# Performance work log

Measured on AMD Instinct MI355X. Metric: run time of the kernel, lower is better.

The kernel has to match this reference:

```python
import jax, jax.numpy as jnp
import numpy as np
from jax import lax

DN = ('NCHW', 'OIHW', 'NCHW')

def conv(x, w, pad='VALID'):
    return lax.conv_general_dilated(x, w, (1, 1), pad, dimension_numbers=DN)

def adaptive_matrix(in_s, out_s):
    # exact torch adaptive_avg_pool2d bin weights: start=floor(i*in/out), end=ceil((i+1)*in/out)
    M = np.zeros((out_s, in_s), np.float32)
    for i in range(out_s):
        s = (i * in_s) // out_s
        e = -(-((i + 1) * in_s) // out_s)
        M[i, s:e] = 1.0 / (e - s)
    return jnp.asarray(M)

def setup_inputs() -> dict:
    key = jax.random.key(0)
    ks = jax.random.split(key, 11)
    C = 64
    def w(k, shape, fan_in):
        return jax.random.normal(k, shape, jnp.float32) * (1.0 / np.sqrt(fan_in))
    return {
        'x': jax.random.normal(ks[0], (16, C, 128, 128), jnp.float32),
        'conv1_w': w(ks[1], (2 * C, C, 1, 1), C),
        'conv1_b': jnp.zeros((2 * C,), jnp.float32),
        'conv2_w': w(ks[2], (C, C, 1, 1), C),
        'conv2_b': jnp.zeros((C,), jnp.float32),
        'conv3_w': w(ks[3], (C, 2 * C, 1, 1), 2 * C),
        'conv3_b': jnp.zeros((C,), jnp.float32),
        'pos_w': w(ks[4], (C, C, 3, 3), C * 9),
        'pos_b': jnp.zeros((C,), jnp.float32),
        'se_w1': w(ks[5], (C // 8, C, 1, 1), C),
        'se_w2': w(ks[6], (C, C // 8, 1, 1), C // 8),
    }

def reference(x, conv1_w, conv1_b, conv2_w, conv2_b, conv3_w, conv3_b, pos_w, pos_b, se_w1, se_w2):
    C, nw, ext = 64, 4, 4
    y = conv(x, conv1_w) + conv1_b[None, :, None, None]
    x1, x2 = y[:, :C], y[:, C:]
    N, _, H, W = x1.shape
    x1p = jnp.pad(x1, ((0, 0), (0, 0), (ext, ext), (ext, ext)), mode='edge')
    Hp, Wp = H + 2 * ext, W + 2 * ext
    Hs, Ws = H // nw, W // nw
    Hk, Wk = Hs + H % nw, Ws + W % nw
    Hps, Wps = Hp // nw, Wp // nw
    Hpk, Wpk = Hps + Hp % nw, Wps + Wp % nw
    # unfold: windows row-major (h_window fastest over j), shape (N, nw^2, C, Hpk, Wpk)
    wins = jnp.stack([x1p[:, :, i * Hps:i * Hps + Hpk, j * Wps:j * Wps + Wpk]
                      for i in range(nw) for j in range(nw)], axis=1)
    Ph = adaptive_matrix(Hpk, Hk)
    Pw = adaptive_matrix(Wpk, Wk)
    pooled = jnp.einsum('nlchw,Hh,Ww->nlcHW', wins, Ph, Pw).reshape(N * nw * nw, C, Hk, Wk)
    pr = (conv(pooled, conv2_w) + conv2_b[None, :, None, None]
          + conv(pooled, pos_w, 'SAME') + pos_b[None, :, None, None])
    # SE attention
    s = jnp.mean(pr, axis=(2, 3), keepdims=True)
    s = jax.nn.sigmoid(conv(jax.nn.relu(conv(s, se_w1)), se_w2))
    att = pr * s + pr
    # faithful torch .view(N, C*Hk*Wk, nw^2) memory reinterpretation, then fold
    cols = att.reshape(N, nw * nw * C * Hk * Wk).reshape(N, C, Hk, Wk, nw * nw)
    out = jnp.zeros((N, C, H, W), x.dtype)
    cnt = jnp.zeros((N, 1, H, W), x.dtype)
    for i in range(nw):
        for j in range(nw):
            l = i * nw + j
            out = out.at[:, :, i * Hs:i * Hs + Hk, j * Ws:j * Ws + Wk].add(cols[..., l])
            cnt = cnt.at[:, :, i * Hs:i * Hs + Hk, j * Ws:j * Ws + Wk].add(1.0)
    out = out / cnt
    return conv(jnp.concatenate([out, x2], axis=1), conv3_w) + conv3_b[None, :, None, None]
```

## Files before the change

kernel.cpp:

```cpp
#include <hip/hip_runtime.h>

constexpr int N = 16, C = 64, H = 128, W = 128, P = H * W;
constexpr int NL = 256, PK = 1024;

constexpr size_t OFF_RA    = 0;
constexpr size_t OFF_RB    = 8388608;
constexpr size_t OFF_RC    = 16777216;
constexpr size_t OFF_SUMS  = 33554432;
constexpr size_t OFF_SCALE = OFF_SUMS  + 16384;
constexpr size_t OFF_WMOD  = OFF_SCALE + 16384;
constexpr size_t OFF_W1L   = OFF_WMOD  + 18432;
constexpr size_t OFF_W3L   = OFF_W1L   + 4096;

typedef short bf16x8 __attribute__((ext_vector_type(8)));
typedef float f32x4  __attribute__((ext_vector_type(4)));

__device__ inline unsigned short f2bf(float f) {
    unsigned u = __float_as_uint(f);
    unsigned r = (u + 0x7FFFu + ((u >> 16) & 1u)) >> 16;
    return (unsigned short)r;
}
__device__ inline float bf2f(unsigned short h) {
    return __uint_as_float(((unsigned)h) << 16);
}

__global__ __launch_bounds__(256) void k0_prep(const float* __restrict__ pos_w,
                                               const float* __restrict__ conv2_w,
                                               const float* __restrict__ w1,
                                               const float* __restrict__ w3,
                                               unsigned short* __restrict__ wmod,
                                               unsigned short* __restrict__ w1lay,
                                               unsigned short* __restrict__ w3lay,
                                               float* __restrict__ sums) {
    int t = blockIdx.x * 256 + threadIdx.x;
    if (t < 36864) {
        int cir = t & 31;
        int co  = (t >> 5) & 63;
        int cib = (t >> 11) & 1;
        int tap = t >> 12;
        int ci  = cib * 32 + cir;
        float v = pos_w[(co * 64 + ci) * 9 + tap];
        if (tap == 4) v += conv2_w[co * 64 + ci];
        wmod[t] = f2bf(v);
    } else if (t < 45056) {
        int u = t - 36864;
        int cir = u & 31;
        int co  = (u >> 5) & 127;
        int cib = u >> 12;
        w1lay[u] = f2bf(w1[co * 64 + cib * 32 + cir]);
    } else if (t < 53248) {
        int u = t - 45056;
        int cir = u & 31;
        int co  = (u >> 5) & 63;
        int cib = u >> 11;
        w3lay[u] = f2bf(w3[co * 128 + cib * 32 + cir]);
    } else {
        sums[t - 53248] = 0.f;
    }
}

__global__ __launch_bounds__(256) void k1_conv1(const float* __restrict__ x,
                                                const unsigned short* __restrict__ w1lay,
                                                const float* __restrict__ b1,
                                                unsigned short* __restrict__ x1t,
                                                unsigned short* __restrict__ xcat) {
    __shared__ __align__(16) float lda[64 * 65];
    __shared__ __align__(16) unsigned short ldb[128 * 64];
    int bid = blockIdx.x;
    int n   = bid >> 7;
    int px0 = (bid & 127) << 7;
    int t   = threadIdx.x;
    #pragma unroll
    for (int s = 0; s < 2; ++s) {
        if (s) __syncthreads();
        const float* src = x + (size_t)n * 64 * P + px0 + s * 64;
        #pragma unroll
        for (int k = 0; k < 4; ++k) {
            int u = t + k * 256;
            int ci = u >> 4, px4 = u & 15;
            float4 v = *(const float4*)(src + (size_t)ci * P + px4 * 4);
            float* d = lda + ci * 65 + px4 * 4;
            d[0] = v.x; d[1] = v.y; d[2] = v.z; d[3] = v.w;
        }
        __syncthreads();
        int cig = t & 15, pxl = t >> 4;
        #pragma unroll
        for (int k = 0; k < 4; ++k) {
            int px = pxl + k * 16;
            ushort4 o;
            o.x = f2bf(lda[(cig * 4 + 0) * 65 + px]);
            o.y = f2bf(lda[(cig * 4 + 1) * 65 + px]);
            o.z = f2bf(lda[(cig * 4 + 2) * 65 + px]);
            o.w = f2bf(lda[(cig * 4 + 3) * 65 + px]);
            int pg = s * 64 + px;
            int chunk = cig >> 1;
            *(ushort4*)(ldb + pg * 64 + ((chunk ^ (pg & 7)) * 8) + (cig & 1) * 4) = o;
        }
    }
    __syncthreads();
    int wave = t >> 6, lane = t & 63;
    int quad = lane >> 4, l16 = lane & 15;
    int pxw = wave * 32;
    f32x4 acc[8][2] = {};
    #pragma unroll
    for (int cib = 0; cib < 2; ++cib) {
        bf16x8 af[8], bfr[2];
        #pragma unroll
        for (int ct = 0; ct < 8; ++ct)
            af[ct] = *(const bf16x8*)(w1lay + ((size_t)(cib * 128 + ct * 16 + l16)) * 32 + quad * 8);
        #pragma unroll
        for (int pt = 0; pt < 2; ++pt) {
            int pg = pxw + pt * 16 + l16;
            int chunk = cib * 4 + quad;
            bfr[pt] = *(const bf16x8*)(ldb + pg * 64 + ((chunk ^ (pg & 7)) * 8));
        }
        #pragma unroll
        for (int ct = 0; ct < 8; ++ct)
            #pragma unroll
            for (int pt = 0; pt < 2; ++pt)
                acc[ct][pt] = __builtin_amdgcn_mfma_f32_16x16x32_bf16(af[ct], bfr[pt], acc[ct][pt], 0, 0, 0);
    }
    #pragma unroll
    for (int ct = 0; ct < 8; ++ct) {
        int co0 = ct * 16 + quad * 4;
        float4 bb = *(const float4*)(b1 + co0);
        #pragma unroll
        for (int pt = 0; pt < 2; ++pt) {
            int px = px0 + pxw + pt * 16 + l16;
            ushort4 o;
            o.x = f2bf(acc[ct][pt][0] + bb.x);
            o.y = f2bf(acc[ct][pt][1] + bb.y);
            o.z = f2bf(acc[ct][pt][2] + bb.z);
            o.w = f2bf(acc[ct][pt][3] + bb.w);
            if (co0 < 64)
                *(ushort4*)(x1t + ((size_t)n * P + px) * 64 + co0) = o;
            else
                *(ushort4*)(xcat + ((size_t)n * P + px) * 128 + co0) = o;
        }
    }
}

__global__ __launch_bounds__(256) void k3_pool_pr(const unsigned short* __restrict__ x1t,
                                                  const unsigned short* __restrict__ wmod,
                                                  const float* __restrict__ b2,
                                                  const float* __restrict__ posb,
                                                  unsigned short* __restrict__ prb,
                                                  float* __restrict__ sums) {
    __shared__ __align__(16) unsigned short lxs[340 * 32];
    int bid = blockIdx.x;
    int nl  = bid >> 2;
    int r0  = (bid & 3) * 8;
    int n   = nl >> 4, wl = nl & 15;
    int wi  = wl >> 2, wj = wl & 3;
    int t   = threadIdx.x;
    const unsigned short* xb = x1t + (size_t)n * P * 64;
    int wave = t >> 6, lane = t & 63;
    int quad = lane >> 4, l16 = lane & 15;
    int wrow0 = wave * 2;
    f32x4 acc[4][4] = {};
    #pragma unroll
    for (int cib = 0; cib < 2; ++cib) {
        if (cib) __syncthreads();
        for (int it = 0; it < 6; ++it) {
            int e = t + it * 256;
            if (e < 1360) {
                int pix = e >> 2, part = e & 3;
                int lr = pix / 34, lc = pix - lr * 34;
                int gr = r0 - 1 + lr, gc = lc - 1;
                unsigned short oc[8];
                if ((unsigned)gr < 32u && (unsigned)gc < 32u) {
                    int sh = gr + (gr >> 4), sw = gc + (gc >> 4);
                    int u = wi * 34 + sh - 4, v = wj * 34 + sw - 4;
                    int ra = min(max(u, 0), 127), rb = min(max(u + 1, 0), 127);
                    int ca = min(max(v, 0), 127), cb = min(max(v + 1, 0), 127);
                    int off = cib * 32 + part * 8;
                    uint4 A = *(const uint4*)(xb + (size_t)(ra * 128 + ca) * 64 + off);
                    uint4 B = *(const uint4*)(xb + (size_t)(ra * 128 + cb) * 64 + off);
                    uint4 Cc = *(const uint4*)(xb + (size_t)(rb * 128 + ca) * 64 + off);
                    uint4 D = *(const uint4*)(xb + (size_t)(rb * 128 + cb) * 64 + off);
                    const unsigned short* a = (const unsigned short*)&A;
                    const unsigned short* b = (const unsigned short*)&B;
                    const unsigned short* c = (const unsigned short*)&Cc;
                    const unsigned short* d = (const unsigned short*)&D;
                    #pragma unroll
                    for (int q = 0; q < 8; ++q)
                        oc[q] = f2bf(0.25f * (bf2f(a[q]) + bf2f(b[q]) + bf2f(c[q]) + bf2f(d[q])));
                } else {
                    #pragma unroll
                    for (int q = 0; q < 8; ++q) oc[q] = 0;
                }
                *(uint4*)(lxs + pix * 32 + ((part ^ ((pix >> 1) & 3)) * 8)) = *(const uint4*)oc;
            }
        }
        __syncthreads();
        #pragma unroll
        for (int tap = 0; tap < 9; ++tap) {
            int dh = tap / 3, dw = tap % 3;
            bf16x8 af[4], bfr[4];
            #pragma unroll
            for (int ct = 0; ct < 4; ++ct)
                af[ct] = *(const bf16x8*)(wmod + (((tap * 2 + cib) * 64) + ct * 16 + l16) * 32 + quad * 8);
            #pragma unroll
            for (int pt = 0; pt < 4; ++pt) {
                int pix = (wrow0 + (pt >> 1) + dh) * 34 + ((pt & 1) * 16 + l16 + dw);
                bfr[pt] = *(const bf16x8*)(lxs + pix * 32 + ((quad ^ ((pix >> 1) & 3)) * 8));
            }
            #pragma unroll
            for (int ct = 0; ct < 4; ++ct)
                #pragma unroll
                for (int pt = 0; pt < 4; ++pt)
                    acc[ct][pt] = __builtin_amdgcn_mfma_f32_16x16x32_bf16(af[ct], bfr[pt], acc[ct][pt], 0, 0, 0);
        }
    }
    #pragma unroll
    for (int ct = 0; ct < 4; ++ct) {
        #pragma unroll
        for (int r = 0; r < 4; ++r) {
            int co = ct * 16 + quad * 4 + r;
            float bias = b2[co] + posb[co];
            float s = 0.f;
            #pragma unroll
            for (int pt = 0; pt < 4; ++pt) {
                float v = acc[ct][pt][r] + bias;
                int row = r0 + wrow0 + (pt >> 1);
                int col = (pt & 1) * 16 + l16;
                prb[(size_t)nl * 65536 + co * 1024 + row * 32 + col] = f2bf(v);
                s += v;
            }
            s += __shfl_xor(s, 1);
            s += __shfl_xor(s, 2);
            s += __shfl_xor(s, 4);
            s += __shfl_xor(s, 8);
            if (l16 == 0) atomicAdd(&sums[nl * 64 + co], s);
        }
    }
}

__global__ __launch_bounds__(64) void k3b_se(const float* __restrict__ sums,
                                             const float* __restrict__ w1,
                                             const float* __restrict__ w2,
                                             float* __restrict__ scale) {
    __shared__ float m[64];
    __shared__ float hid[8];
    int nl = blockIdx.x;
    int t  = threadIdx.x;
    m[t] = sums[nl * 64 + t] * (1.f / 1024.f);
    __syncthreads();
    if (t < 8) {
        float s = 0.f;
        #pragma unroll
        for (int ci = 0; ci < 64; ++ci) s += w1[t * 64 + ci] * m[ci];
        hid[t] = fmaxf(s, 0.f);
    }
    __syncthreads();
    float v = 0.f;
    #pragma unroll
    for (int r = 0; r < 8; ++r) v += w2[t * 8 + r] * hid[r];
    scale[nl * 64 + t] = 1.f + 1.f / (1.f + __expf(-v));
}

__global__ __launch_bounds__(256) void k4_unscramble(const unsigned short* __restrict__ prb,
                                                     const float* __restrict__ scale,
                                                     unsigned short* __restrict__ xcat) {
    int tid = blockIdx.x * 256 + threadIdx.x;
    int cg = tid & 7;
    int w2 = (tid >> 3) & 31;
    int h2 = (tid >> 8) & 31;
    int i  = (tid >> 13) & 3;
    int n  = tid >> 15;
    int hh = (h2 & 1) * 16 + (w2 >> 1);
    int pixbase = hh * 32 + (w2 & 1) * 16 + i * 4;
    unsigned short o[4][8];
    #pragma unroll
    for (int m = 0; m < 8; ++m) {
        int c  = cg * 8 + m;
        int nl = n * 16 + (c >> 2);
        int cc = (c & 3) * 16 + (h2 >> 1);
        ushort4 v = *(const ushort4*)(prb + (size_t)nl * 65536 + cc * 1024 + pixbase);
        float s = scale[nl * 64 + cc];
        o[0][m] = f2bf(bf2f(v.x) * s);
        o[1][m] = f2bf(bf2f(v.y) * s);
        o[2][m] = f2bf(bf2f(v.z) * s);
        o[3][m] = f2bf(bf2f(v.w) * s);
    }
    int H_ = i * 32 + h2;
    #pragma unroll
    for (int j = 0; j < 4; ++j) {
        int W_ = j * 32 + w2;
        *(uint4*)(xcat + ((size_t)n * P + H_ * 128 + W_) * 128 + cg * 8) = *(const uint4*)o[j];
    }
}

__global__ __launch_bounds__(256) void k5_conv3(const unsigned short* __restrict__ xcat,
                                                const unsigned short* __restrict__ w3lay,
                                                const float* __restrict__ b3,
                                                float* __restrict__ out) {
    __shared__ __align__(16) unsigned short lxs[128 * 136];
    int bid = blockIdx.x;
    int n   = bid >> 7;
    int px0 = (bid & 127) << 7;
    const unsigned short* src = xcat + ((size_t)n * P + px0) * 128;
    int t = threadIdx.x;
    #pragma unroll
    for (int it = 0; it < 8; ++it) {
        int e = t + it * 256;
        int pix = e >> 4, part = e & 15;
        *(uint4*)(lxs + pix * 136 + part * 8) = *(const uint4*)(src + pix * 128 + part * 8);
    }
    __syncthreads();
    int wave = t >> 6, lane = t & 63;
    int quad = lane >> 4, l16 = lane & 15;
    int pxw = wave * 32;
    f32x4 acc[4][2] = {};
    #pragma unroll
    for (int cib = 0; cib < 4; ++cib) {
        bf16x8 af[4], bfr[2];
        #pragma unroll
        for (int ct = 0; ct < 4; ++ct)
            af[ct] = *(const bf16x8*)(w3lay + ((size_t)(cib * 64 + ct * 16 + l16)) * 32 + quad * 8);
        #pragma unroll
        for (int pt = 0; pt < 2; ++pt)
            bfr[pt] = *(const bf16x8*)(lxs + (pxw + pt * 16 + l16) * 136 + cib * 32 + quad * 8);
        #pragma unroll
        for (int ct = 0; ct < 4; ++ct)
            #pragma unroll
            for (int pt = 0; pt < 2; ++pt)
                acc[ct][pt] = __builtin_amdgcn_mfma_f32_16x16x32_bf16(af[ct], bfr[pt], acc[ct][pt], 0, 0, 0);
    }
    #pragma unroll
    for (int ct = 0; ct < 4; ++ct) {
        int co0 = ct * 16 + quad * 4;
        float4 bb = *(const float4*)(b3 + co0);
        #pragma unroll
        for (int pt = 0; pt < 2; ++pt) {
            int px = px0 + pxw + pt * 16 + l16;
            const float* bp = (const float*)&bb;
            #pragma unroll
            for (int r = 0; r < 4; ++r)
                out[((size_t)n * 64 + co0 + r) * P + px] = acc[ct][pt][r] + bp[r];
        }
    }
}

extern "C" void kernel_launch(void* const* d_in, const int* in_sizes, int n_in,
                              void* d_out, int out_size, void* d_ws, size_t ws_size,
                              hipStream_t stream) {
    const float* x       = (const float*)d_in[0];
    const float* conv1_w = (const float*)d_in[1];
    const float* conv1_b = (const float*)d_in[2];
    const float* conv2_w = (const float*)d_in[3];
    const float* conv2_b = (const float*)d_in[4];
    const float* conv3_w = (const float*)d_in[5];
    const float* conv3_b = (const float*)d_in[6];
    const float* pos_w   = (const float*)d_in[7];
    const float* pos_b   = (const float*)d_in[8];
    const float* se_w1   = (const float*)d_in[9];
    const float* se_w2   = (const float*)d_in[10];

    float* ws = (float*)d_ws;
    unsigned short* prb  = (unsigned short*)(ws + OFF_RA);
    unsigned short* x1t  = (unsigned short*)(ws + OFF_RB);
    unsigned short* xcat = (unsigned short*)(ws + OFF_RC);
    float* sums  = ws + OFF_SUMS;
    float* scale = ws + OFF_SCALE;
    unsigned short* wmod  = (unsigned short*)(ws + OFF_WMOD);
    unsigned short* w1lay = (unsigned short*)(ws + OFF_W1L);
    unsigned short* w3lay = (unsigned short*)(ws + OFF_W3L);

    k0_prep      <<<272,  256, 0, stream>>>(pos_w, conv2_w, conv1_w, conv3_w,
                                            wmod, w1lay, w3lay, sums);
    k1_conv1     <<<2048, 256, 0, stream>>>(x, w1lay, conv1_b, x1t, xcat);
    k3_pool_pr   <<<1024, 256, 0, stream>>>(x1t, wmod, conv2_b, pos_b, prb, sums);
    k3b_se       <<<256,  64,  0, stream>>>(sums, se_w1, se_w2, scale);
    k4_unscramble<<<2048, 256, 0, stream>>>(prb, scale, xcat);
    k5_conv3     <<<2048, 256, 0, stream>>>(xcat, w3lay, conv3_b, (float*)d_out);
}
```

Baseline: 257.9 us.

## Fuse SE, unscramble and weight prep into neighbouring kernels, cutting launches

Folds weight preparation and sums zeroing into extra blocks of the conv1 kernel. It also fuses the SE scale computation and the fold/unscramble directly into the conv3 kernel, which now gathers the pooled result from prb with scaling instead of going through an xcat buffer. Conv1 now reads x and w1 straight from global memory without LDS staging. The pool kernel stages both channel halves at once with a single barrier. Kernel launches drop from six to three and the xcat round trip is removed, at the cost of uncoalesced scalar gathers in conv1 and conv3 and redundant SE computation per block.

New measurement: 275.1 us. 6.7% more time.

```diff
diff --git a/kernel.cpp b/kernel.cpp
--- a/kernel.cpp
+++ b/kernel.cpp
@@ -3,14 +3,12 @@
 constexpr int N = 16, C = 64, H = 128, W = 128, P = H * W;
 constexpr int NL = 256, PK = 1024;
 
-constexpr size_t OFF_RA    = 0;
-constexpr size_t OFF_RB    = 8388608;
-constexpr size_t OFF_RC    = 16777216;
-constexpr size_t OFF_SUMS  = 33554432;
-constexpr size_t OFF_SCALE = OFF_SUMS  + 16384;
-constexpr size_t OFF_WMOD  = OFF_SCALE + 16384;
-constexpr size_t OFF_W1L   = OFF_WMOD  + 18432;
-constexpr size_t OFF_W3L   = OFF_W1L   + 4096;
+constexpr size_t OFF_RA   = 0;
+constexpr size_t OFF_RB   = 8388608;
+constexpr size_t OFF_RC   = 16777216;
+constexpr size_t OFF_SUMS = 25165824;
+constexpr size_t OFF_WMOD = OFF_SUMS + 16384;
+constexpr size_t OFF_W3L  = OFF_WMOD + 18432;
 
 typedef short bf16x8 __attribute__((ext_vector_type(8)));
 typedef float f32x4  __attribute__((ext_vector_type(4)));
@@ -24,101 +22,67 @@
     return __uint_as_float(((unsigned)h) << 16);
 }
 
-__global__ __launch_bounds__(256) void k0_prep(const float* __restrict__ pos_w,
-                                               const float* __restrict__ conv2_w,
-                                               const float* __restrict__ w1,
-                                               const float* __restrict__ w3,
-                                               unsigned short* __restrict__ wmod,
-                                               unsigned short* __restrict__ w1lay,
-                                               unsigned short* __restrict__ w3lay,
-                                               float* __restrict__ sums) {
-    int t = blockIdx.x * 256 + threadIdx.x;
-    if (t < 36864) {
-        int cir = t & 31;
-        int co  = (t >> 5) & 63;
-        int cib = (t >> 11) & 1;
-        int tap = t >> 12;
-        int ci  = cib * 32 + cir;
-        float v = pos_w[(co * 64 + ci) * 9 + tap];
-        if (tap == 4) v += conv2_w[co * 64 + ci];
-        wmod[t] = f2bf(v);
-    } else if (t < 45056) {
-        int u = t - 36864;
-        int cir = u & 31;
-        int co  = (u >> 5) & 127;
-        int cib = u >> 12;
-        w1lay[u] = f2bf(w1[co * 64 + cib * 32 + cir]);
-    } else if (t < 53248) {
-        int u = t - 45056;
-        int cir = u & 31;
-        int co  = (u >> 5) & 63;
-        int cib = u >> 11;
-        w3lay[u] = f2bf(w3[co * 128 + cib * 32 + cir]);
-    } else {
-        sums[t - 53248] = 0.f;
-    }
-}
-
 __global__ __launch_bounds__(256) void k1_conv1(const float* __restrict__ x,
-                                                const unsigned short* __restrict__ w1lay,
+                                                const float* __restrict__ w1,
                                                 const float* __restrict__ b1,
+                                                const float* __restrict__ pos_w,
+                                                const float* __restrict__ conv2_w,
+                                                const float* __restrict__ w3,
                                                 unsigned short* __restrict__ x1t,
-                                                unsigned short* __restrict__ xcat) {
-    __shared__ __align__(16) float lda[64 * 65];
-    __shared__ __align__(16) unsigned short ldb[128 * 64];
+                                                unsigned short* __restrict__ x2t,
+                                                unsigned short* __restrict__ wmod,
+                                                unsigned short* __restrict__ w3lay,
+                                                float* __restrict__ sums) {
     int bid = blockIdx.x;
-    int n   = bid >> 7;
-    int px0 = (bid & 127) << 7;
     int t   = threadIdx.x;
-    #pragma unroll
-    for (int s = 0; s < 2; ++s) {
-        if (s) __syncthreads();
-        const float* src = x + (size_t)n * 64 * P + px0 + s * 64;
-        #pragma unroll
-        for (int k = 0; k < 4; ++k) {
-            int u = t + k * 256;
-            int ci = u >> 4, px4 = u & 15;
-            float4 v = *(const float4*)(src + (size_t)ci * P + px4 * 4);
-            float* d = lda + ci * 65 + px4 * 4;
-            d[0] = v.x; d[1] = v.y; d[2] = v.z; d[3] = v.w;
-        }
-        __syncthreads();
-        int cig = t & 15, pxl = t >> 4;
-        #pragma unroll
-        for (int k = 0; k < 4; ++k) {
-            int px = pxl + k * 16;
-            ushort4 o;
-            o.x = f2bf(lda[(cig * 4 + 0) * 65 + px]);
-            o.y = f2bf(lda[(cig * 4 + 1) * 65 + px]);
-            o.z = f2bf(lda[(cig * 4 + 2) * 65 + px]);
-            o.w = f2bf(lda[(cig * 4 + 3) * 65 + px]);
-            int pg = s * 64 + px;
-            int chunk = cig >> 1;
-            *(ushort4*)(ldb + pg * 64 + ((chunk ^ (pg & 7)) * 8) + (cig & 1) * 4) = o;
-        }
-    }
-    __syncthreads();
+    if (bid >= 2048) {
+        for (int u = (bid - 2048) * 256 + t; u < 61440; u += 8192) {
+            if (u < 36864) {
+                int cir = u & 31, co = (u >> 5) & 63, cib = (u >> 11) & 1, tap = u >> 12;
+                int ci = cib * 32 + cir;
+                float v = pos_w[(co * 64 + ci) * 9 + tap];
+                if (tap == 4) v += conv2_w[co * 64 + ci];
+                wmod[u] = f2bf(v);
+            } else if (u < 45056) {
+                int q = u - 36864;
+                int cir = q & 31, co = (q >> 5) & 63, cib = q >> 11;
+                w3lay[q] = f2bf(w3[co * 128 + cib * 32 + cir]);
+            } else {
+                sums[u - 45056] = 0.f;
+            }
+        }
+        return;
+    }
+    int n    = bid >> 7;
     int wave = t >> 6, lane = t & 63;
     int quad = lane >> 4, l16 = lane & 15;
-    int pxw = wave * 32;
+    int px0  = (bid & 127) * 128 + wave * 32;
+    const float* xb = x + (size_t)n * 64 * P;
     f32x4 acc[8][2] = {};
     #pragma unroll
     for (int cib = 0; cib < 2; ++cib) {
-        bf16x8 af[8], bfr[2];
-        #pragma unroll
-        for (int ct = 0; ct < 8; ++ct)
-            af[ct] = *(const bf16x8*)(w1lay + ((size_t)(cib * 128 + ct * 16 + l16)) * 32 + quad * 8);
-        #pragma unroll
-        for (int pt = 0; pt < 2; ++pt) {
-            int pg = pxw + pt * 16 + l16;
-            int chunk = cib * 4 + quad;
-            bfr[pt] = *(const bf16x8*)(ldb + pg * 64 + ((chunk ^ (pg & 7)) * 8));
-        }
-        #pragma unroll
-        for (int ct = 0; ct < 8; ++ct)
-            #pragma unroll
-            for (int pt = 0; pt < 2; ++pt)
-                acc[ct][pt] = __builtin_amdgcn_mfma_f32_16x16x32_bf16(af[ct], bfr[pt], acc[ct][pt], 0, 0, 0);
+        bf16x8 bfr[2];
+        #pragma unroll
+        for (int pt = 0; pt < 2; ++pt) {
+            int px = px0 + pt * 16 + l16;
+            unsigned short tmp[8];
+            #pragma unroll
+            for (int j = 0; j < 8; ++j)
+                tmp[j] = f2bf(xb[(size_t)(cib * 32 + quad * 8 + j) * P + px]);
+            bfr[pt] = *(bf16x8*)tmp;
+        }
+        #pragma unroll
+        for (int ct = 0; ct < 8; ++ct) {
+            const float* wr = w1 + (ct * 16 + l16) * 64 + cib * 32 + quad * 8;
+            float4 wa = *(const float4*)wr;
+            float4 wb = *(const float4*)(wr + 4);
+            unsigned short wt[8];
+            wt[0] = f2bf(wa.x); wt[1] = f2bf(wa.y); wt[2] = f2bf(wa.z); wt[3] = f2bf(wa.w);
+            wt[4] = f2bf(wb.x); wt[5] = f2bf(wb.y); wt[6] = f2bf(wb.z); wt[7] = f2bf(wb.w);
+            bf16x8 af = *(bf16x8*)wt;
+            acc[ct][0] = __builtin_amdgcn_mfma_f32_16x16x32_bf16(af, bfr[0], acc[ct][0], 0, 0, 0);
+            acc[ct][1] = __builtin_amdgcn_mfma_f32_16x16x32_bf16(af, bfr[1], acc[ct][1], 0, 0, 0);
+        }
     }
     #pragma unroll
     for (int ct = 0; ct < 8; ++ct) {
@@ -126,7 +90,7 @@
         float4 bb = *(const float4*)(b1 + co0);
         #pragma unroll
         for (int pt = 0; pt < 2; ++pt) {
-            int px = px0 + pxw + pt * 16 + l16;
+            int px = px0 + pt * 16 + l16;
             ushort4 o;
             o.x = f2bf(acc[ct][pt][0] + bb.x);
             o.y = f2bf(acc[ct][pt][1] + bb.y);
@@ -135,7 +99,7 @@
             if (co0 < 64)
                 *(ushort4*)(x1t + ((size_t)n * P + px) * 64 + co0) = o;
             else
-                *(ushort4*)(xcat + ((size_t)n * P + px) * 128 + co0) = o;
+                *(ushort4*)(x2t + ((size_t)n * P + px) * 64 + (co0 - 64)) = o;
         }
     }
 }
@@ -146,7 +110,7 @@
                                                   const float* __restrict__ posb,
                                                   unsigned short* __restrict__ prb,
                                                   float* __restrict__ sums) {
-    __shared__ __align__(16) unsigned short lxs[340 * 32];
+    __shared__ __align__(16) unsigned short lxs[2 * 340 * 32];
     int bid = blockIdx.x;
     int nl  = bid >> 2;
     int r0  = (bid & 3) * 8;
@@ -154,48 +118,50 @@
     int wi  = wl >> 2, wj = wl & 3;
     int t   = threadIdx.x;
     const unsigned short* xb = x1t + (size_t)n * P * 64;
+    for (int it = 0; it < 11; ++it) {
+        int e = t + it * 256;
+        if (e < 2720) {
+            int part = e & 3;
+            int u    = e >> 2;
+            int cib  = (u >= 340);
+            int pix  = u - cib * 340;
+            int lr = pix / 34, lc = pix - lr * 34;
+            int gr = r0 - 1 + lr, gc = lc - 1;
+            unsigned short oc[8];
+            if ((unsigned)gr < 32u && (unsigned)gc < 32u) {
+                int sh = gr + (gr >> 4), sw = gc + (gc >> 4);
+                int uu = wi * 34 + sh - 4, vv = wj * 34 + sw - 4;
+                int ra = min(max(uu, 0), 127), rb = min(max(uu + 1, 0), 127);
+                int ca = min(max(vv, 0), 127), cb = min(max(vv + 1, 0), 127);
+                int off = cib * 32 + part * 8;
+                uint4 A  = *(const uint4*)(xb + (size_t)(ra * 128 + ca) * 64 + off);
+                uint4 B  = *(const uint4*)(xb + (size_t)(ra * 128 + cb) * 64 + off);
+                uint4 Cc = *(const uint4*)(xb + (size_t)(rb * 128 + ca) * 64 + off);
+                uint4 D  = *(const uint4*)(xb + (size_t)(rb * 128 + cb) * 64 + off);
+                const unsigned short* a = (const unsigned short*)&A;
+                const unsigned short* b = (const unsigned short*)&B;
+                const unsigned short* c = (const unsigned short*)&Cc;
+                const unsigned short* d = (const unsigned short*)&D;
+                #pragma unroll
+                for (int q = 0; q < 8; ++q)
+                    oc[q] = f2bf(0.25f * (bf2f(a[q]) + bf2f(b[q]) + bf2f(c[q]) + bf2f(d[q])));
+            } else {
+                #pragma unroll
+                for (int q = 0; q < 8; ++q) oc[q] = 0;
+            }
+            *(uint4*)(lxs + cib * 10880 + pix * 32 + ((part ^ ((pix >> 1) & 3)) * 8)) = *(const uint4*)oc;
+        }
+    }
+    __syncthreads();
     int wave = t >> 6, lane = t & 63;
     int quad = lane >> 4, l16 = lane & 15;
     int wrow0 = wave * 2;
     f32x4 acc[4][4] = {};
     #pragma unroll
-    for (int cib = 0; cib < 2; ++cib) {
-        if (cib) __syncthreads();
-        for (int it = 0; it < 6; ++it) {
-            int e = t + it * 256;
-            if (e < 1360) {
-                int pix = e >> 2, part = e & 3;
-                int lr = pix / 34, lc = pix - lr * 34;
-                int gr = r0 - 1 + lr, gc = lc - 1;
-                unsigned short oc[8];
-                if ((unsigned)gr < 32u && (unsigned)gc < 32u) {
-                    int sh = gr + (gr >> 4), sw = gc + (gc >> 4);
-                    int u = wi * 34 + sh - 4, v = wj * 34 + sw - 4;
-                    int ra = min(max(u, 0), 127), rb = min(max(u + 1, 0), 127);
-                    int ca = min(max(v, 0), 127), cb = min(max(v + 1, 0), 127);
-                    int off = cib * 32 + part * 8;
-                    uint4 A = *(const uint4*)(xb + (size_t)(ra * 128 + ca) * 64 + off);
-                    uint4 B = *(const uint4*)(xb + (size_t)(ra * 128 + cb) * 64 + off);
-                    uint4 Cc = *(const uint4*)(xb + (size_t)(rb * 128 + ca) * 64 + off);
-                    uint4 D = *(const uint4*)(xb + (size_t)(rb * 128 + cb) * 64 + off);
-                    const unsigned short* a = (const unsigned short*)&A;
-                    const unsigned short* b = (const unsigned short*)&B;
-                    const unsigned short* c = (const unsigned short*)&Cc;
-                    const unsigned short* d = (const unsigned short*)&D;
-                    #pragma unroll
-                    for (int q = 0; q < 8; ++q)
-                        oc[q] = f2bf(0.25f * (bf2f(a[q]) + bf2f(b[q]) + bf2f(c[q]) + bf2f(d[q])));
-                } else {
-                    #pragma unroll
-                    for (int q = 0; q < 8; ++q) oc[q] = 0;
-                }
-                *(uint4*)(lxs + pix * 32 + ((part ^ ((pix >> 1) & 3)) * 8)) = *(const uint4*)oc;
-            }
-        }
-        __syncthreads();
-        #pragma unroll
-        for (int tap = 0; tap < 9; ++tap) {
-            int dh = tap / 3, dw = tap % 3;
+    for (int tap = 0; tap < 9; ++tap) {
+        int dh = tap / 3, dw = tap % 3;
+        #pragma unroll
+        for (int cib = 0; cib < 2; ++cib) {
             bf16x8 af[4], bfr[4];
             #pragma unroll
             for (int ct = 0; ct < 4; ++ct)
@@ -203,7 +169,7 @@
             #pragma unroll
             for (int pt = 0; pt < 4; ++pt) {
                 int pix = (wrow0 + (pt >> 1) + dh) * 34 + ((pt & 1) * 16 + l16 + dw);
-                bfr[pt] = *(const bf16x8*)(lxs + pix * 32 + ((quad ^ ((pix >> 1) & 3)) * 8));
+                bfr[pt] = *(const bf16x8*)(lxs + cib * 10880 + pix * 32 + ((quad ^ ((pix >> 1) & 3)) * 8));
             }
             #pragma unroll
             for (int ct = 0; ct < 4; ++ct)
@@ -236,108 +202,96 @@
     }
 }
 
-__global__ __launch_bounds__(64) void k3b_se(const float* __restrict__ sums,
-                                             const float* __restrict__ w1,
-                                             const float* __restrict__ w2,
-                                             float* __restrict__ scale) {
-    __shared__ float m[64];
-    __shared__ float hid[8];
-    int nl = blockIdx.x;
-    int t  = threadIdx.x;
-    m[t] = sums[nl * 64 + t] * (1.f / 1024.f);
-    __syncthreads();
-    if (t < 8) {
-        float s = 0.f;
-        #pragma unroll
-        for (int ci = 0; ci < 64; ++ci) s += w1[t * 64 + ci] * m[ci];
-        hid[t] = fmaxf(s, 0.f);
-    }
-    __syncthreads();
-    float v = 0.f;
-    #pragma unroll
-    for (int r = 0; r < 8; ++r) v += w2[t * 8 + r] * hid[r];
-    scale[nl * 64 + t] = 1.f + 1.f / (1.f + __expf(-v));
-}
-
-__global__ __launch_bounds__(256) void k4_unscramble(const unsigned short* __restrict__ prb,
-                                                     const float* __restrict__ scale,
-                                                     unsigned short* __restrict__ xcat) {
-    int tid = blockIdx.x * 256 + threadIdx.x;
-    int cg = tid & 7;
-    int w2 = (tid >> 3) & 31;
-    int h2 = (tid >> 8) & 31;
-    int i  = (tid >> 13) & 3;
-    int n  = tid >> 15;
-    int hh = (h2 & 1) * 16 + (w2 >> 1);
-    int pixbase = hh * 32 + (w2 & 1) * 16 + i * 4;
-    unsigned short o[4][8];
-    #pragma unroll
-    for (int m = 0; m < 8; ++m) {
-        int c  = cg * 8 + m;
-        int nl = n * 16 + (c >> 2);
-        int cc = (c & 3) * 16 + (h2 >> 1);
-        ushort4 v = *(const ushort4*)(prb + (size_t)nl * 65536 + cc * 1024 + pixbase);
-        float s = scale[nl * 64 + cc];
-        o[0][m] = f2bf(bf2f(v.x) * s);
-        o[1][m] = f2bf(bf2f(v.y) * s);
-        o[2][m] = f2bf(bf2f(v.z) * s);
-        o[3][m] = f2bf(bf2f(v.w) * s);
-    }
-    int H_ = i * 32 + h2;
-    #pragma unroll
-    for (int j = 0; j < 4; ++j) {
-        int W_ = j * 32 + w2;
-        *(uint4*)(xcat + ((size_t)n * P + H_ * 128 + W_) * 128 + cg * 8) = *(const uint4*)o[j];
-    }
-}
-
-__global__ __launch_bounds__(256) void k5_conv3(const unsigned short* __restrict__ xcat,
+__global__ __launch_bounds__(256) void k5_conv3(const unsigned short* __restrict__ prb,
+                                                const float* __restrict__ sums,
+                                                const float* __restrict__ se_w1,
+                                                const float* __restrict__ se_w2,
+                                                const unsigned short* __restrict__ x2t,
                                                 const unsigned short* __restrict__ w3lay,
                                                 const float* __restrict__ b3,
                                                 float* __restrict__ out) {
-    __shared__ __align__(16) unsigned short lxs[128 * 136];
-    int bid = blockIdx.x;
-    int n   = bid >> 7;
-    int px0 = (bid & 127) << 7;
-    const unsigned short* src = xcat + ((size_t)n * P + px0) * 128;
-    int t = threadIdx.x;
-    #pragma unroll
-    for (int it = 0; it < 8; ++it) {
-        int e = t + it * 256;
-        int pix = e >> 4, part = e & 15;
-        *(uint4*)(lxs + pix * 136 + part * 8) = *(const uint4*)(src + pix * 128 + part * 8);
+    __shared__ float shid[16][8];
+    __shared__ float sscale[64];
+    int bid  = blockIdx.x;
+    int n    = bid >> 7;
+    int Hrow = bid & 127;
+    int h2 = Hrow & 31, ib = Hrow >> 5;
+    int t  = threadIdx.x;
+    if (t < 128) {
+        int lam = t >> 3, r = t & 7;
+        const float* sp = sums + (n * 16 + lam) * 64;
+        float s = 0.f;
+        #pragma unroll
+        for (int ci = 0; ci < 64; ++ci) s += se_w1[r * 64 + ci] * sp[ci];
+        shid[lam][r] = fmaxf(s * (1.f / 1024.f), 0.f);
+    }
+    __syncthreads();
+    if (t < 64) {
+        int lam = t >> 2, q = t & 3;
+        int cc = q * 16 + (h2 >> 1);
+        float v = 0.f;
+        #pragma unroll
+        for (int r = 0; r < 8; ++r) v += se_w2[cc * 8 + r] * shid[lam][r];
+        sscale[t] = 1.f + 1.f / (1.f + __expf(-v));
     }
     __syncthreads();
     int wave = t >> 6, lane = t & 63;
     int quad = lane >> 4, l16 = lane & 15;
-    int pxw = wave * 32;
     f32x4 acc[4][2] = {};
     #pragma unroll
-    for (int cib = 0; cib < 4; ++cib) {
-        bf16x8 af[4], bfr[2];
-        #pragma unroll
-        for (int ct = 0; ct < 4; ++ct)
-            af[ct] = *(const bf16x8*)(w3lay + ((size_t)(cib * 64 + ct * 16 + l16)) * 32 + quad * 8);
-        #pragma unroll
-        for (int pt = 0; pt < 2; ++pt)
-            bfr[pt] = *(const bf16x8*)(lxs + (pxw + pt * 16 + l16) * 136 + cib * 32 + quad * 8);
-        #pragma unroll
-        for (int ct = 0; ct < 4; ++ct)
+    for (int cib = 0; cib < 2; ++cib) {
+        bf16x8 bfr[2];
+        #pragma unroll
+        for (int pt = 0; pt < 2; ++pt) {
+            int Wp = wave * 32 + pt * 16 + l16;
+            int w2 = Wp & 31, jW = Wp >> 5;
+            int hh  = (h2 & 1) * 16 + (w2 >> 1);
+            int pix = hh * 32 + (w2 & 1) * 16 + ib * 4 + jW;
+            unsigned short tmp[8];
+            #pragma unroll
+            for (int j = 0; j < 8; ++j) {
+                int c  = cib * 32 + quad * 8 + j;
+                int nl = n * 16 + (c >> 2);
+                int cc = (c & 3) * 16 + (h2 >> 1);
+                tmp[j] = f2bf(bf2f(prb[(size_t)nl * 65536 + cc * 1024 + pix]) * sscale[c]);
+            }
+            bfr[pt] = *(bf16x8*)tmp;
+        }
+        #pragma unroll
+        for (int ct = 0; ct < 4; ++ct) {
+            bf16x8 af = *(const bf16x8*)(w3lay + ((size_t)(cib * 64 + ct * 16 + l16)) * 32 + quad * 8);
             #pragma unroll
             for (int pt = 0; pt < 2; ++pt)
-                acc[ct][pt] = __builtin_amdgcn_mfma_f32_16x16x32_bf16(af[ct], bfr[pt], acc[ct][pt], 0, 0, 0);
+                acc[ct][pt] = __builtin_amdgcn_mfma_f32_16x16x32_bf16(af, bfr[pt], acc[ct][pt], 0, 0, 0);
+        }
+    }
+    #pragma unroll
+    for (int cb = 0; cb < 2; ++cb) {
+        bf16x8 bfr[2];
+        #pragma unroll
+        for (int pt = 0; pt < 2; ++pt) {
+            int Wp = wave * 32 + pt * 16 + l16;
+            bfr[pt] = *(const bf16x8*)(x2t + ((size_t)n * P + Hrow * 128 + Wp) * 64 + cb * 32 + quad * 8);
+        }
+        #pragma unroll
+        for (int ct = 0; ct < 4; ++ct) {
+            bf16x8 af = *(const bf16x8*)(w3lay + ((size_t)((2 + cb) * 64 + ct * 16 + l16)) * 32 + quad * 8);
+            #pragma unroll
+            for (int pt = 0; pt < 2; ++pt)
+                acc[ct][pt] = __builtin_amdgcn_mfma_f32_16x16x32_bf16(af, bfr[pt], acc[ct][pt], 0, 0, 0);
+        }
     }
     #pragma unroll
     for (int ct = 0; ct < 4; ++ct) {
         int co0 = ct * 16 + quad * 4;
         float4 bb = *(const float4*)(b3 + co0);
-        #pragma unroll
-        for (int pt = 0; pt < 2; ++pt) {
-            int px = px0 + pxw + pt * 16 + l16;
-            const float* bp = (const float*)&bb;
+        const float* bp = (const float*)&bb;
+        #pragma unroll
+        for (int pt = 0; pt < 2; ++pt) {
+            int Wp = wave * 32 + pt * 16 + l16;
             #pragma unroll
             for (int r = 0; r < 4; ++r)
-                out[((size_t)n * 64 + co0 + r) * P + px] = acc[ct][pt][r] + bp[r];
+                out[((size_t)n * 64 + co0 + r) * P + Hrow * 128 + Wp] = acc[ct][pt][r] + bp[r];
         }
     }
 }
@@ -360,18 +314,14 @@
     float* ws = (float*)d_ws;
     unsigned short* prb  = (unsigned short*)(ws + OFF_RA);
     unsigned short* x1t  = (unsigned short*)(ws + OFF_RB);
-    unsigned short* xcat = (unsigned short*)(ws + OFF_RC);
-    float* sums  = ws + OFF_SUMS;
-    float* scale = ws + OFF_SCALE;
+    unsigned short* x2t  = (unsigned short*)(ws + OFF_RC);
+    float* sums = ws + OFF_SUMS;
     unsigned short* wmod  = (unsigned short*)(ws + OFF_WMOD);
-    unsigned short* w1lay = (unsigned short*)(ws + OFF_W1L);
     unsigned short* w3lay = (unsigned short*)(ws + OFF_W3L);
 
-    k0_prep      <<<272,  256, 0, stream>>>(pos_w, conv2_w, conv1_w, conv3_w,
-                                            wmod, w1lay, w3lay, sums);
-    k1_conv1     <<<2048, 256, 0, stream>>>(x, w1lay, conv1_b, x1t, xcat);
-    k3_pool_pr   <<<1024, 256, 0, stream>>>(x1t, wmod, conv2_b, pos_b, prb, sums);
-    k3b_se       <<<256,  64,  0, stream>>>(sums, se_w1, se_w2, scale);
-    k4_unscramble<<<2048, 256, 0, stream>>>(prb, scale, xcat);
-    k5_conv3     <<<2048, 256, 0, stream>>>(xcat, w3lay, conv3_b, (float*)d_out);
-}
+    k1_conv1  <<<2080, 256, 0, stream>>>(x, conv1_w, conv1_b, pos_w, conv2_w, conv3_w,
+                                         x1t, x2t, wmod, w3lay, sums);
+    k3_pool_pr<<<1024, 256, 0, stream>>>(x1t, wmod, conv2_b, pos_b, prb, sums);
+    k5_conv3  <<<2048, 256, 0, stream>>>(prb, sums, se_w1, se_w2, x2t, w3lay,
+                                         conv3_b, (float*)d_out);
+}
```
